# Optimization experiments

Measured on AMD Instinct MI355X. Metric: run time of the kernel, lower is better.

Reference implementation:

```python
import jax, jax.numpy as jnp
import numpy as np

N0, N1, N2 = 16384, 4096, 1024   # node counts at the 3 hierarchy levels
DEG = 16                          # avg degree -> E = N*DEG per level
OUT_CH = 4
GTD = 2048                        # global_token_dim


def _gcn(x, ei, w, b):
    # GCNConv: out = D^{-1/2} (A + I) D^{-1/2} (x @ W) + b
    n = x.shape[0]
    h = x @ w
    loop = jnp.arange(n, dtype=ei.dtype)
    src = jnp.concatenate([ei[0], loop])
    dst = jnp.concatenate([ei[1], loop])
    deg = jax.ops.segment_sum(jnp.ones(src.shape[0], h.dtype), dst, num_segments=n)
    dinv = jax.lax.rsqrt(jnp.maximum(deg, 1.0))   # deg >= 1 thanks to self loops
    coef = (dinv[src] * dinv[dst])[:, None]
    return jax.ops.segment_sum(h[src] * coef, dst, num_segments=n) + b


def _knn_interp(x, pos_src, pos_dst, k):
    # inverse-squared-distance weighted interpolation over k nearest sources
    d2 = (jnp.sum(pos_dst * pos_dst, -1, keepdims=True)
          + jnp.sum(pos_src * pos_src, -1)[None, :]
          - 2.0 * (pos_dst @ pos_src.T))          # (M, N) squared distances
    negd, idx = jax.lax.top_k(-d2, k)
    w = 1.0 / jnp.maximum(-negd, 1e-16)           # (M, k)
    return jnp.einsum('mk,mkc->mc', w, x[idx]) / jnp.sum(w, -1, keepdims=True)


def _bnorm(h, gamma, beta):
    # BatchNorm1d in training mode (batch statistics over nodes)
    mu = jnp.mean(h, 0)
    var = jnp.mean((h - mu) ** 2, 0)
    return (h - mu) * jax.lax.rsqrt(var + 1e-5) * gamma + beta


def _forward(fl, idx0, idx1, ei0, ei1, ei2):
    (x, pos,
     s1w0, s1b0, s1w1, s1b1, s1w2, s1b2,
     s2w0, s2b0, s2w1, s2b1, s2w2, s2b2,
     bw0, bb0, bw1, bb1, bw2, bb2,
     gw0, gb0, gw1, gb1, gw2, gb2, gg0, gbe0, gg1, gbe1,
     f2w0, f2b0, f2w1, f2b1, f2w2, f2b2,
     f1w0, f1b0, f1w1, f1b1, f1w2, f1b2,
     mw0, mb0, mw1, mb1) = fl
    relu = jax.nn.relu
    # SA1 (skip_pos_encoding=True): convs on full graph, then subsample by idx0
    h = relu(_gcn(x, ei0, s1w0, s1b0))
    h = relu(_gcn(h, ei0, s1w1, s1b1))
    h = relu(_gcn(h, ei0, s1w2, s1b2))
    x1, pos1 = h[idx0], pos[idx0]                 # (N1, 64)
    # SA2: concat pos, convs on level-1 graph, subsample by idx1
    h = jnp.concatenate([x1, pos1], 1)
    h = relu(_gcn(h, ei1, s2w0, s2b0))
    h = relu(_gcn(h, ei1, s2w1, s2b1))
    h = relu(_gcn(h, ei1, s2w2, s2b2))
    x2, pos2 = h[idx1], pos1[idx1]                # (N2, 128)
    # bottleneck (no subsample)
    h = jnp.concatenate([x2, pos2], 1)
    h = relu(_gcn(h, ei2, bw0, bb0))
    h = relu(_gcn(h, ei2, bw1, bb1))
    xb = relu(_gcn(h, ei2, bw2, bb2))             # (N2, 256)
    # GlobalSA: MLP(+BN) -> global max pool -> k=1 interp (broadcast, B=1) -> concat skip
    g = jnp.concatenate([x2, pos2], 1)
    g = relu(_bnorm(g @ gw0 + gb0, gg0, gbe0))
    g = relu(_bnorm(g @ gw1 + gb1, gg1, gbe1))
    g = g @ gw2 + gb2                             # (N2, GTD)
    gmax = jnp.max(g, 0, keepdims=True)
    h = jnp.concatenate([jnp.broadcast_to(gmax, (x2.shape[0], gmax.shape[1])), xb], 1)
    # FP2: knn-interpolate level2 -> level1, concat skip, convs on level-1 graph
    h = _knn_interp(h, pos2, pos1, 3)
    h = jnp.concatenate([h, x1], 1)               # (N1, GTD+256+64)
    h = relu(_gcn(h, ei1, f2w0, f2b0))
    h = relu(_gcn(h, ei1, f2w1, f2b1))
    h = relu(_gcn(h, ei1, f2w2, f2b2))
    # FP1: knn-interpolate level1 -> level0, concat raw features, convs on full graph
    h = _knn_interp(h, pos1, pos, 3)
    h = jnp.concatenate([h, x], 1)                # (N0, 518)
    h = relu(_gcn(h, ei0, f1w0, f1b0))
    h = relu(_gcn(h, ei0, f1w1, f1b1))
    h = relu(_gcn(h, ei0, f1w2, f1b2))            # (N0, 128)
    # final MLP (norm=None)
    return relu(h @ mw0 + mb0) @ mw1 + mb1        # (N0, OUT_CH)


def setup_inputs() -> dict:
    keys = iter(jax.random.split(jax.random.key(0), 64))
    def lin(i, o):
        return (jax.random.normal(next(keys), (i, o), jnp.float32) / np.float32(np.sqrt(i)),
                jnp.zeros((o,), jnp.float32))
    d = {}
    d['x'] = jax.random.normal(next(keys), (N0, 6), jnp.float32)
    d['pos'] = jax.random.uniform(next(keys), (N0, 3), jnp.float32)
    for nm, sp in [('sa1', [(6, 32), (32, 32), (32, 64)]),
                   ('sa2', [(67, 64), (64, 64), (64, 128)]),
                   ('bn', [(131, 128), (128, 128), (128, 256)])]:
        for j, (i, o) in enumerate(sp):
            d[nm + '_w' + str(j)], d[nm + '_b' + str(j)] = lin(i, o)
    for j, (i, o) in enumerate([(131, 512), (512, 1024), (1024, GTD)]):
        d['g_w' + str(j)], d['g_b' + str(j)] = lin(i, o)
    d['g_g0'] = jnp.ones((512,), jnp.float32); d['g_be0'] = jnp.zeros((512,), jnp.float32)
    d['g_g1'] = jnp.ones((1024,), jnp.float32); d['g_be1'] = jnp.zeros((1024,), jnp.float32)
    for nm, sp in [('fp2', [(GTD + 256 + 64, 1024), (1024, 1024), (1024, 512)]),
                   ('fp1', [(512 + 6, 256), (256, 256), (256, 128)])]:
        for j, (i, o) in enumerate(sp):
            d[nm + '_w' + str(j)], d[nm + '_b' + str(j)] = lin(i, o)
    d['m_w0'], d['m_b0'] = lin(128, 64)
    d['m_w1'], d['m_b1'] = lin(64, OUT_CH)
    d['idx0'] = jax.random.randint(next(keys), (N1,), 0, N0)
    d['idx1'] = jax.random.randint(next(keys), (N2,), 0, N1)
    d['ei0'] = jax.random.randint(next(keys), (2, N0 * DEG), 0, N0)
    d['ei1'] = jax.random.randint(next(keys), (2, N1 * DEG), 0, N1)
    d['ei2'] = jax.random.randint(next(keys), (2, N2 * DEG), 0, N2)
    return d


def reference(x, pos,
              sa1_w0, sa1_b0, sa1_w1, sa1_b1, sa1_w2, sa1_b2,
              sa2_w0, sa2_b0, sa2_w1, sa2_b1, sa2_w2, sa2_b2,
              bn_w0, bn_b0, bn_w1, bn_b1, bn_w2, bn_b2,
              g_w0, g_b0, g_w1, g_b1, g_w2, g_b2, g_g0, g_be0, g_g1, g_be1,
              fp2_w0, fp2_b0, fp2_w1, fp2_b1, fp2_w2, fp2_b2,
              fp1_w0, fp1_b0, fp1_w1, fp1_b1, fp1_w2, fp1_b2,
              m_w0, m_b0, m_w1, m_b1,
              idx0, idx1, ei0, ei1, ei2):
    fl = (x, pos,
          sa1_w0, sa1_b0, sa1_w1, sa1_b1, sa1_w2, sa1_b2,
          sa2_w0, sa2_b0, sa2_w1, sa2_b1, sa2_w2, sa2_b2,
          bn_w0, bn_b0, bn_w1, bn_b1, bn_w2, bn_b2,
          g_w0, g_b0, g_w1, g_b1, g_w2, g_b2, g_g0, g_be0, g_g1, g_be1,
          fp2_w0, fp2_b0, fp2_w1, fp2_b1, fp2_w2, fp2_b2,
          fp1_w0, fp1_b0, fp1_w1, fp1_b1, fp1_w2, fp1_b2,
          m_w0, m_b0, m_w1, m_b1)
    return _forward(fl, idx0, idx1, ei0, ei1, ei2)
```

## Files before the change

kernel.cpp:

```cpp
#include <hip/hip_runtime.h>
#include <hip/hip_bf16.h>

typedef __hip_bfloat16 bf16;
typedef __attribute__((ext_vector_type(8))) short bf8v;
typedef __attribute__((ext_vector_type(4))) float f32x4;

__device__ __forceinline__ float ldw(const void* p, long i, int isbf) {
    return isbf ? __bfloat162float(((const bf16*)p)[i]) : ((const float*)p)[i];
}
__device__ __forceinline__ unsigned short f2bf(float v) {
    bf16 h = __float2bfloat16(v);
    return *reinterpret_cast<unsigned short*>(&h);
}
__device__ __forceinline__ float bfu2f(unsigned short u) {
    return __uint_as_float((unsigned)u << 16);
}

__global__ void k_detect(const unsigned short* __restrict__ w, int n, int* __restrict__ flag) {
    __shared__ int cnt;
    if (threadIdx.x == 0) cnt = 0;
    __syncthreads();
    int bad = 0;
    for (int i = threadIdx.x; i < n; i += 256) {
        int e = (w[i] >> 7) & 0xFF;
        if (e == 0xFF || (e != 0 && (e < 64 || e > 190))) bad++;
    }
    atomicAdd(&cnt, bad);
    __syncthreads();
    if (threadIdx.x == 0) *flag = (cnt > n / 16) ? 0 : 1;
}

__global__ void k_cvt_in(const void* __restrict__ s, float* __restrict__ d, int n,
                         const int* __restrict__ flag) {
    int i = blockIdx.x * 256 + threadIdx.x;
    if (i < n) d[i] = ldw(s, i, *flag);
}
__global__ void k_out(const float* __restrict__ s, void* __restrict__ d, int n,
                      const int* __restrict__ flag) {
    int i = blockIdx.x * 256 + threadIdx.x;
    if (i < n) {
        if (*flag) ((bf16*)d)[i] = __float2bfloat16(s[i]);
        else       ((float*)d)[i] = s[i];
    }
}
__global__ void k_zero(float* __restrict__ d, int n) {
    int i = blockIdx.x * 256 + threadIdx.x;
    if (i < n) d[i] = 0.f;
}
__global__ void k_zero_i(int* __restrict__ d, int n) {
    int i = blockIdx.x * 256 + threadIdx.x;
    if (i < n) d[i] = 0;
}

__global__ void k_count(const int* __restrict__ dst, int* __restrict__ cnt, int E) {
    int i = blockIdx.x * 256 + threadIdx.x;
    if (i < E) atomicAdd(&cnt[dst[i]], 1);
}
__global__ void k_dinv_i(const int* __restrict__ cnt, float* __restrict__ dinv, int n) {
    int i = blockIdx.x * 256 + threadIdx.x;
    if (i < n) dinv[i] = rsqrtf((float)cnt[i] + 1.0f);
}
__global__ __launch_bounds__(1024) void k_scan(const int* __restrict__ cnt,
                                               int* __restrict__ offs, int n) {
    __shared__ int sm[1024];
    int t = threadIdx.x;
    int chunk = (n + 1023) >> 10;
    int b0 = t * chunk, b1 = min(b0 + chunk, n);
    int s = 0;
    for (int i = b0; i < b1; i++) s += cnt[i];
    sm[t] = s;
    __syncthreads();
    for (int o = 1; o < 1024; o <<= 1) {
        int v = (t >= o) ? sm[t - o] : 0;
        __syncthreads();
        sm[t] += v;
        __syncthreads();
    }
    int run = sm[t] - s;
    for (int i = b0; i < b1; i++) { offs[i] = run; run += cnt[i]; }
    if (t == 1023) offs[n] = sm[1023];
}
__global__ void k_fill(const int* __restrict__ src, const int* __restrict__ dst,
                       const int* __restrict__ offs, int* __restrict__ cur,
                       int* __restrict__ bkt, int E) {
    int e = blockIdx.x * 256 + threadIdx.x;
    if (e < E) {
        int d = dst[e];
        int p = atomicAdd(&cur[d], 1);
        bkt[offs[d] + p] = src[e];
    }
}

__global__ __launch_bounds__(256) void k_wt(const void* __restrict__ W, long woff,
                                            unsigned short* __restrict__ WTh,
                                            unsigned short* __restrict__ WTl,
                                            int K, int N, int Kpad,
                                            const int* __restrict__ flag) {
    __shared__ unsigned short th[32][33];
    __shared__ unsigned short tl[32][33];
    const int isbf = *flag;
    int n0 = blockIdx.x * 32, k0 = blockIdx.y * 32;
    int c = threadIdx.x & 31, r = threadIdx.x >> 5;
    #pragma unroll
    for (int u = 0; u < 4; u++) {
        int k = k0 + r + u * 8;
        float v = (k < K) ? ldw(W, woff + (long)k * N + n0 + c, isbf) : 0.f;
        unsigned short h = f2bf(v);
        th[r + u * 8][c] = h;
        tl[r + u * 8][c] = f2bf(v - bfu2f(h));
    }
    __syncthreads();
    #pragma unroll
    for (int u = 0; u < 4; u++) {
        int n = n0 + r + u * 8;
        WTh[(long)n * Kpad + k0 + c] = th[c][r + u * 8];
        WTl[(long)n * Kpad + k0 + c] = tl[c][r + u * 8];
    }
}

__global__ __launch_bounds__(256) void k_mm(
    const float* __restrict__ A, const void* __restrict__ Wt,
    const void* __restrict__ bias, const float* __restrict__ radd,
    const float* __restrict__ rsc, const float* __restrict__ rs,
    float* __restrict__ C, int M, int K, int N, long woff, int relu,
    const int* __restrict__ flag)
{
    __shared__ float As[2][16][68];
    __shared__ float Bs[2][16][68];
    const int isbf = *flag;
    const int tid = threadIdx.x;
    const int tx = tid & 15, ty = tid >> 4;
    const int bx = blockIdx.x, by = blockIdx.y;

    const int ar = tid >> 2, aq = (tid & 3) << 2;
    const long arow = (long)(by * 64 + ar) * K;
    const int bkk = tid >> 4, bn4 = (tid & 15) << 2;
    const int bcol0 = bx * 64 + bn4;

    float acc[4][4] = {};
    float4 pa, pb;

    auto loadAB = [&](int k0) {
        int kg = k0 + aq;
        pa.x = (kg + 0 < K) ? A[arow + kg + 0] : 0.f;
        pa.y = (kg + 1 < K) ? A[arow + kg + 1] : 0.f;
        pa.z = (kg + 2 < K) ? A[arow + kg + 2] : 0.f;
        pa.w = (kg + 3 < K) ? A[arow + kg + 3] : 0.f;
        int kb = k0 + bkk;
        pb = make_float4(0.f, 0.f, 0.f, 0.f);
        if (kb < K) {
            long base = woff + (long)kb * N + bcol0;
            if (bcol0 + 3 < N) {
                pb.x = ldw(Wt, base + 0, isbf); pb.y = ldw(Wt, base + 1, isbf);
                pb.z = ldw(Wt, base + 2, isbf); pb.w = ldw(Wt, base + 3, isbf);
            } else {
                if (bcol0 < N)     pb.x = ldw(Wt, base + 0, isbf);
                if (bcol0 + 1 < N) pb.y = ldw(Wt, base + 1, isbf);
                if (bcol0 + 2 < N) pb.z = ldw(Wt, base + 2, isbf);
            }
        }
    };
    auto storeAB = [&](int b) {
        As[b][aq + 0][ar] = pa.x;  As[b][aq + 1][ar] = pa.y;
        As[b][aq + 2][ar] = pa.z;  As[b][aq + 3][ar] = pa.w;
        *(float4*)&Bs[b][bkk][bn4] = pb;
    };

    loadAB(0);
    storeAB(0);
    __syncthreads();

    const int nk = (K + 15) >> 4;
    for (int t = 0; t < nk; t++) {
        const int cur = t & 1;
        const bool more = (t + 1 < nk);
        if (more) loadAB((t + 1) << 4);
        #pragma unroll
        for (int kk = 0; kk < 16; kk++) {
            float4 a = *(const float4*)&As[cur][kk][ty << 2];
            float4 b = *(const float4*)&Bs[cur][kk][tx << 2];
            float av[4] = {a.x, a.y, a.z, a.w};
            float bv[4] = {b.x, b.y, b.z, b.w};
            #pragma unroll
            for (int i = 0; i < 4; i++)
                #pragma unroll
                for (int j = 0; j < 4; j++)
                    acc[i][j] = fmaf(av[i], bv[j], acc[i][j]);
        }
        if (more) storeAB(cur ^ 1);
        __syncthreads();
    }

    const int col = bx * 64 + (tx << 2);
    #pragma unroll
    for (int i = 0; i < 4; i++) {
        int r = by * 64 + (ty << 2) + i;
        float m = rs ? rs[r] : 1.0f;
        float rr = rsc ? rsc[r] : 1.0f;
        float v[4];
        #pragma unroll
        for (int j = 0; j < 4; j++) {
            v[j] = acc[i][j] * m;
            int c = col + j;
            if (c < N) {
                if (bias) v[j] += ldw(bias, c, isbf);
                if (radd) v[j] += radd[c] * rr;
            }
            if (relu) v[j] = fmaxf(v[j], 0.f);
        }
        if (col + 3 < N) {
            float4 o = {v[0], v[1], v[2], v[3]};
            *(float4*)&C[(long)r * N + col] = o;
        } else {
            for (int j = 0; j < 4; j++)
                if (col + j < N) C[(long)r * N + col + j] = v[j];
        }
    }
}

__global__ __launch_bounds__(256, 4) void k_mmx(
    const float* __restrict__ A,
    const unsigned short* __restrict__ WTh, const unsigned short* __restrict__ WTl,
    const void* __restrict__ bias, const float* __restrict__ radd,
    const float* __restrict__ rsc, const float* __restrict__ rs,
    float* __restrict__ C, int M, int K, int Kpad, int N, int relu,
    const int* __restrict__ flag)
{
    __shared__ unsigned short Ash[64][72];
    __shared__ unsigned short Asl[64][72];
    __shared__ unsigned short Bsh[64][72];
    __shared__ unsigned short Bsl[64][72];
    const int tid = threadIdx.x;
    const int bx = blockIdx.x, by = blockIdx.y;
    const int lane = tid & 63, wid = tid >> 6;
    const int wr = wid >> 1, wc = wid & 1;
    const int lr = lane & 15, lg = lane >> 4;
    const int ar = tid >> 2, aq = (tid & 3) << 4;
    const long arow = (long)(by * 64 + ar) * K;
    const unsigned short* wrh = WTh + (long)(bx * 64 + ar) * Kpad;
    const unsigned short* wrl = WTl + (long)(bx * 64 + ar) * Kpad;

    f32x4 acc00 = {0,0,0,0}, acc01 = {0,0,0,0};
    f32x4 acc10 = {0,0,0,0}, acc11 = {0,0,0,0};
    bf8v pah0, pah1, pal0, pal1, pbh0, pbh1, pbl0, pbl1;

    auto ld = [&](int k0) {
        int kg = k0 + aq;
        float va[16];
        if (kg + 16 <= K) {
            if ((K & 3) == 0) {
                #pragma unroll
                for (int q = 0; q < 4; q++)
                    *(float4*)&va[4 * q] = *(const float4*)&A[arow + kg + 4 * q];
            } else if ((K & 1) == 0) {
                #pragma unroll
                for (int q = 0; q < 8; q++)
                    *(float2*)&va[2 * q] = *(const float2*)&A[arow + kg + 2 * q];
            } else {
                #pragma unroll
                for (int e = 0; e < 16; e++) va[e] = A[arow + kg + e];
            }
        } else {
            #pragma unroll
            for (int e = 0; e < 16; e++) va[e] = (kg + e < K) ? A[arow + kg + e] : 0.f;
        }
        #pragma unroll
        for (int e = 0; e < 8; e++) {
            unsigned short h = f2bf(va[e]);
            pah0[e] = (short)h;
            pal0[e] = (short)f2bf(va[e] - bfu2f(h));
        }
        #pragma unroll
        for (int e = 0; e < 8; e++) {
            unsigned short h = f2bf(va[8 + e]);
            pah1[e] = (short)h;
            pal1[e] = (short)f2bf(va[8 + e] - bfu2f(h));
        }
        pbh0 = *(const bf8v*)(wrh + kg);
        pbh1 = *(const bf8v*)(wrh + kg + 8);
        pbl0 = *(const bf8v*)(wrl + kg);
        pbl1 = *(const bf8v*)(wrl + kg + 8);
    };

    ld(0);
    for (int k0 = 0; k0 < K; k0 += 64) {
        __syncthreads();
        *(bf8v*)&Ash[ar][aq] = pah0;  *(bf8v*)&Ash[ar][aq + 8] = pah1;
        *(bf8v*)&Asl[ar][aq] = pal0;  *(bf8v*)&Asl[ar][aq + 8] = pal1;
        *(bf8v*)&Bsh[ar][aq] = pbh0;  *(bf8v*)&Bsh[ar][aq + 8] = pbh1;
        *(bf8v*)&Bsl[ar][aq] = pbl0;  *(bf8v*)&Bsl[ar][aq + 8] = pbl1;
        __syncthreads();
        if (k0 + 64 < K) ld(k0 + 64);
        #pragma unroll
        for (int ks = 0; ks < 2; ks++) {
            int kb = ks * 32 + lg * 8;
            bf8v a0h = *(const bf8v*)&Ash[wr * 32 + lr][kb];
            bf8v a1h = *(const bf8v*)&Ash[wr * 32 + 16 + lr][kb];
            bf8v a0l = *(const bf8v*)&Asl[wr * 32 + lr][kb];
            bf8v a1l = *(const bf8v*)&Asl[wr * 32 + 16 + lr][kb];
            bf8v b0h = *(const bf8v*)&Bsh[wc * 32 + lr][kb];
            bf8v b1h = *(const bf8v*)&Bsh[wc * 32 + 16 + lr][kb];
            bf8v b0l = *(const bf8v*)&Bsl[wc * 32 + lr][kb];
            bf8v b1l = *(const bf8v*)&Bsl[wc * 32 + 16 + lr][kb];
            acc00 = __builtin_amdgcn_mfma_f32_16x16x32_bf16(a0l, b0h, acc00, 0, 0, 0);
            acc00 = __builtin_amdgcn_mfma_f32_16x16x32_bf16(a0h, b0l, acc00, 0, 0, 0);
            acc00 = __builtin_amdgcn_mfma_f32_16x16x32_bf16(a0h, b0h, acc00, 0, 0, 0);
            acc01 = __builtin_amdgcn_mfma_f32_16x16x32_bf16(a0l, b1h, acc01, 0, 0, 0);
            acc01 = __builtin_amdgcn_mfma_f32_16x16x32_bf16(a0h, b1l, acc01, 0, 0, 0);
            acc01 = __builtin_amdgcn_mfma_f32_16x16x32_bf16(a0h, b1h, acc01, 0, 0, 0);
            acc10 = __builtin_amdgcn_mfma_f32_16x16x32_bf16(a1l, b0h, acc10, 0, 0, 0);
            acc10 = __builtin_amdgcn_mfma_f32_16x16x32_bf16(a1h, b0l, acc10, 0, 0, 0);
            acc10 = __builtin_amdgcn_mfma_f32_16x16x32_bf16(a1h, b0h, acc10, 0, 0, 0);
            acc11 = __builtin_amdgcn_mfma_f32_16x16x32_bf16(a1l, b1h, acc11, 0, 0, 0);
            acc11 = __builtin_amdgcn_mfma_f32_16x16x32_bf16(a1h, b1l, acc11, 0, 0, 0);
            acc11 = __builtin_amdgcn_mfma_f32_16x16x32_bf16(a1h, b1h, acc11, 0, 0, 0);
        }
    }

    const int isbf = *flag;
    const int rb = by * 64 + wr * 32, cb = bx * 64 + wc * 32;
    auto epi = [&](f32x4 a, int mf, int nf) {
        int col = cb + nf * 16 + lr;
        float bv = bias ? ldw(bias, col, isbf) : 0.f;
        float rv = radd ? radd[col] : 0.f;
        #pragma unroll
        for (int g = 0; g < 4; g++) {
            int row = rb + mf * 16 + lg * 4 + g;
            float v = a[g] * (rs ? rs[row] : 1.f) + bv
                    + rv * (rsc ? rsc[row] : 1.f);
            if (relu) v = fmaxf(v, 0.f);
            C[(long)row * N + col] = v;
        }
    };
    epi(acc00, 0, 0); epi(acc01, 0, 1); epi(acc10, 1, 0); epi(acc11, 1, 1);
}

__global__ __launch_bounds__(256) void k_aggr(const float* __restrict__ t,
    const int* __restrict__ offs, const int* __restrict__ bkt,
    const float* __restrict__ dinv, const void* __restrict__ bias,
    float* __restrict__ out, int n, int C, int relu, const int* __restrict__ flag)
{
    const int G = C >> 2;
    long i = blockIdx.x * 256L + threadIdx.x;
    if (i >= (long)n * G) return;
    int d = (int)(i / G), g = (int)(i % G);
    const float4* t4 = (const float4*)t;
    float4 acc = t4[(long)d * G + g];
    int o0 = offs[d], o1 = offs[d + 1];
    for (int j = o0; j < o1; j++) {
        int s = bkt[j];
        float4 v = t4[(long)s * G + g];
        acc.x += v.x; acc.y += v.y; acc.z += v.z; acc.w += v.w;
    }
    float dd = dinv[d];
    acc.x *= dd; acc.y *= dd; acc.z *= dd; acc.w *= dd;
    if (bias) {
        int isbf = *flag; int c = g << 2;
        acc.x += ldw(bias, c, isbf); acc.y += ldw(bias, c + 1, isbf);
        acc.z += ldw(bias, c + 2, isbf); acc.w += ldw(bias, c + 3, isbf);
    }
    if (relu) {
        acc.x = fmaxf(acc.x, 0.f); acc.y = fmaxf(acc.y, 0.f);
        acc.z = fmaxf(acc.z, 0.f); acc.w = fmaxf(acc.w, 0.f);
    }
    ((float4*)out)[(long)d * G + g] = acc;
}

__global__ void k_rowmul(float* __restrict__ h, const float* __restrict__ s, int n, int C) {
    long i = blockIdx.x * 256L + threadIdx.x;
    if (i < (long)n * C) h[i] *= s[i / C];
}
__global__ void k_sigacc(const int* __restrict__ src, const int* __restrict__ dst,
                         const float* __restrict__ dinv, float* __restrict__ sig, int E) {
    int e = blockIdx.x * 256 + threadIdx.x;
    if (e < E) atomicAdd(&sig[dst[e]], dinv[src[e]]);
}
__global__ void k_sigfin(float* __restrict__ sig, const float* __restrict__ dinv, int n) {
    int i = blockIdx.x * 256 + threadIdx.x;
    if (i < n) sig[i] = dinv[i] * (sig[i] + dinv[i]);
}
__global__ void k_rowvec_acc(const float* __restrict__ gmax, const void* __restrict__ W,
                             float* __restrict__ out, const int* __restrict__ flag) {
    int n = blockIdx.x * 256 + threadIdx.x;
    if (n >= 1024) return;
    const int isbf = *flag;
    int c0 = blockIdx.y * 128;
    float s = 0.f;
    for (int c = c0; c < c0 + 128; c++) s += gmax[c] * ldw(W, (long)c * 1024 + n, isbf);
    atomicAdd(&out[n], s);
}

__global__ __launch_bounds__(256) void k_bn(float* __restrict__ h, const void* __restrict__ gamma,
                                            const void* __restrict__ beta, int n, int C,
                                            const int* __restrict__ flag) {
    int c = blockIdx.x;
    int tid = threadIdx.x;
    __shared__ float sm[256];
    float v[4];
    float s = 0.f;
    #pragma unroll
    for (int u = 0; u < 4; u++) {
        int r = tid + u * 256;
        v[u] = (r < n) ? h[(long)r * C + c] : 0.f;
        s += v[u];
    }
    sm[tid] = s; __syncthreads();
    for (int o = 128; o > 0; o >>= 1) { if (tid < o) sm[tid] += sm[tid + o]; __syncthreads(); }
    float mu = sm[0] / n;
    __syncthreads();
    float s2 = 0.f;
    #pragma unroll
    for (int u = 0; u < 4; u++) {
        int r = tid + u * 256;
        if (r < n) { float d = v[u] - mu; s2 += d * d; }
    }
    sm[tid] = s2; __syncthreads();
    for (int o = 128; o > 0; o >>= 1) { if (tid < o) sm[tid] += sm[tid + o]; __syncthreads(); }
    float var = sm[0] / n;
    float rsq = rsqrtf(var + 1e-5f);
    float g = ldw(gamma, c, *flag), be = ldw(beta, c, *flag);
    #pragma unroll
    for (int u = 0; u < 4; u++) {
        int r = tid + u * 256;
        if (r < n) h[(long)r * C + c] = fmaxf((v[u] - mu) * rsq * g + be, 0.f);
    }
}

__global__ __launch_bounds__(256) void k_cmax(const float* __restrict__ h, float* __restrict__ out) {
    __shared__ float sm[256];
    int coff = threadIdx.x & 63, rq = threadIdx.x >> 6;
    int c = blockIdx.x * 64 + coff;
    float m = -3.0e38f;
    for (int r = rq; r < 1024; r += 4) m = fmaxf(m, h[(long)r * 2048 + c]);
    sm[threadIdx.x] = m;
    __syncthreads();
    if (rq == 0) {
        m = fmaxf(fmaxf(sm[coff], sm[64 + coff]), fmaxf(sm[128 + coff], sm[192 + coff]));
        out[c] = m;
    }
}

__global__ void k_gather(const float* __restrict__ src, const int* __restrict__ idx,
                         float* __restrict__ dst, int n, int ncol, int ss, int ds, int doff) {
    long i = blockIdx.x * 256L + threadIdx.x;
    if (i < (long)n * ncol) {
        int r = (int)(i / ncol), c = (int)(i % ncol);
        dst[(long)r * ds + doff + c] = src[(long)idx[r] * ss + c];
    }
}
__global__ void k_copy(const float* __restrict__ src, float* __restrict__ dst,
                       int n, int ncol, int ss, int ds, int doff) {
    long i = blockIdx.x * 256L + threadIdx.x;
    if (i < (long)n * ncol) {
        int r = (int)(i / ncol), c = (int)(i % ncol);
        dst[(long)r * ds + doff + c] = src[(long)r * ss + c];
    }
}

__device__ __forceinline__ bool knn_better(float d, int i, float D, int I) {
    return d < D || (d == D && i < I);
}
__global__ __launch_bounds__(256) void k_knn_w(const float* __restrict__ pdst,
                                               const float* __restrict__ psrc,
                                               int M, int Ns,
                                               int* __restrict__ kidx, float* __restrict__ kw) {
    int wid = (blockIdx.x * 256 + threadIdx.x) >> 6;
    int lane = threadIdx.x & 63;
    if (wid >= M) return;
    float x = pdst[wid * 3], y = pdst[wid * 3 + 1], z = pdst[wid * 3 + 2];
    float nd = x * x + y * y + z * z;
    float bd0 = 3.4e38f, bd1 = 3.4e38f, bd2 = 3.4e38f;
    int bi0 = 0x7fffffff, bi1 = 0x7fffffff, bi2 = 0x7fffffff;
    for (int s = lane; s < Ns; s += 64) {
        float sx = psrc[3 * s], sy = psrc[3 * s + 1], sz = psrc[3 * s + 2];
        float ns = sx * sx + sy * sy + sz * sz;
        float d2 = nd + ns - 2.0f * (x * sx + y * sy + z * sz);
        if (d2 < bd2) {
            if (d2 < bd0)      { bd2 = bd1; bi2 = bi1; bd1 = bd0; bi1 = bi0; bd0 = d2; bi0 = s; }
            else if (d2 < bd1) { bd2 = bd1; bi2 = bi1; bd1 = d2; bi1 = s; }
            else               { bd2 = d2; bi2 = s; }
        }
    }
    #pragma unroll
    for (int off = 32; off >= 1; off >>= 1) {
        float od0 = __shfl_xor(bd0, off, 64); int oi0 = __shfl_xor(bi0, off, 64);
        float od1 = __shfl_xor(bd1, off, 64); int oi1 = __shfl_xor(bi1, off, 64);
        float od2 = __shfl_xor(bd2, off, 64); int oi2 = __shfl_xor(bi2, off, 64);
        float dq[3] = {od0, od1, od2}; int iq[3] = {oi0, oi1, oi2};
        #pragma unroll
        for (int q = 0; q < 3; q++) {
            float dd = dq[q]; int ii = iq[q];
            if (knn_better(dd, ii, bd0, bi0))      { bd2 = bd1; bi2 = bi1; bd1 = bd0; bi1 = bi0; bd0 = dd; bi0 = ii; }
            else if (knn_better(dd, ii, bd1, bi1)) { bd2 = bd1; bi2 = bi1; bd1 = dd; bi1 = ii; }
            else if (knn_better(dd, ii, bd2, bi2)) { bd2 = dd; bi2 = ii; }
        }
    }
    if (lane == 0) {
        kidx[wid * 3] = bi0; kidx[wid * 3 + 1] = bi1; kidx[wid * 3 + 2] = bi2;
        kw[wid * 3]     = 1.0f / fmaxf(bd0, 1e-16f);
        kw[wid * 3 + 1] = 1.0f / fmaxf(bd1, 1e-16f);
        kw[wid * 3 + 2] = 1.0f / fmaxf(bd2, 1e-16f);
    }
}

__global__ void k_knn_apply4(const float* __restrict__ h, const int* __restrict__ kidx,
                             const float* __restrict__ kw, float* __restrict__ out,
                             int M, int C, int ds) {
    const int G = C >> 2;
    long i = blockIdx.x * 256L + threadIdx.x;
    if (i >= (long)M * G) return;
    int r = (int)(i / G), g = (int)(i % G);
    int i0 = kidx[r * 3], i1 = kidx[r * 3 + 1], i2 = kidx[r * 3 + 2];
    float w0 = kw[r * 3], w1 = kw[r * 3 + 1], w2 = kw[r * 3 + 2];
    float inv = 1.0f / (w0 + w1 + w2);
    const float4* h4 = (const float4*)h;
    float4 a = h4[(long)i0 * G + g], b = h4[(long)i1 * G + g], c = h4[(long)i2 * G + g];
    float4 o;
    o.x = (w0 * a.x + w1 * b.x + w2 * c.x) * inv;
    o.y = (w0 * a.y + w1 * b.y + w2 * c.y) * inv;
    o.z = (w0 * a.z + w1 * b.z + w2 * c.z) * inv;
    o.w = (w0 * a.w + w1 * b.w + w2 * c.w) * inv;
    *(float4*)&out[(long)r * ds + (g << 2)] = o;
}
__global__ void k_knn_apply2(const float* __restrict__ h, const int* __restrict__ kidx,
                             const float* __restrict__ kw, float* __restrict__ out,
                             int M, int C, int ds) {
    const int G = C >> 1;
    long i = blockIdx.x * 256L + threadIdx.x;
    if (i >= (long)M * G) return;
    int r = (int)(i / G), g = (int)(i % G);
    int i0 = kidx[r * 3], i1 = kidx[r * 3 + 1], i2 = kidx[r * 3 + 2];
    float w0 = kw[r * 3], w1 = kw[r * 3 + 1], w2 = kw[r * 3 + 2];
    float inv = 1.0f / (w0 + w1 + w2);
    const float2* h2 = (const float2*)h;
    float2 a = h2[(long)i0 * G + g], b = h2[(long)i1 * G + g], c = h2[(long)i2 * G + g];
    float2 o;
    o.x = (w0 * a.x + w1 * b.x + w2 * c.x) * inv;
    o.y = (w0 * a.y + w1 * b.y + w2 * c.y) * inv;
    *(float2*)&out[(long)r * ds + (g << 1)] = o;
}

extern "C" void kernel_launch(void* const* d_in, const int* in_sizes, int n_in,
                              void* d_out, int out_size, void* d_ws, size_t ws_size,
                              hipStream_t stream) {
    const int N0 = 16384, N1 = 4096, N2 = 1024;
    const int E0 = in_sizes[48] / 2, E1 = in_sizes[49] / 2, E2 = in_sizes[50] / 2;

    const int* idx0 = (const int*)d_in[46];
    const int* idx1 = (const int*)d_in[47];
    const int* ei0  = (const int*)d_in[48];
    const int* ei1  = (const int*)d_in[49];
    const int* ei2  = (const int*)d_in[50];

    float* W = (float*)d_ws;
    size_t off = 0;
    auto alloc = [&](size_t nf) { float* p = W + off; off += (nf + 63) & ~(size_t)63; return p; };
    auto allocU = [&](size_t nu) { return (unsigned short*)alloc((nu + 1) / 2); };
    float* P     = alloc(4194304);
    float* Q     = alloc(4194304);
    float* CAT   = alloc(8486912);
    float* xf    = alloc(98304);
    float* posf  = alloc(49152);
    float* pos1  = alloc(12288);
    float* pos2  = alloc(3072);
    float* dinv0 = alloc(16384);
    float* dinv1 = alloc(4096);
    float* dinv2 = alloc(1024);
    float* x1    = alloc(262144);
    float* c2    = alloc(134144);
    float* xb    = alloc(262144);
    float* gmaxb = alloc(2048);
    float* rowv  = alloc(1024);
    float* sigb  = alloc(4096);
    float* kwb   = alloc(49152);
    int*   kib   = (int*)alloc(49152);
    int*   flg   = (int*)alloc(64);
    int*   cntb  = (int*)alloc(16384);
    int*   offs0 = (int*)alloc(16448);
    int*   offs1 = (int*)alloc(4160);
    int*   offs2 = (int*)alloc(1088);
    int*   bkt0  = (int*)alloc(E0);
    int*   bkt1  = (int*)alloc(E1);
    int*   bkt2  = (int*)alloc(E2);

    struct WtPair { unsigned short *h, *l; int Kp; };
    auto mkwt = [&](size_t n, int Kp) {
        WtPair p; p.h = allocU(n); p.l = allocU(n); p.Kp = Kp; return p;
    };
    WtPair wt6  = mkwt(64 * 64, 64);
    WtPair wt8  = mkwt(64 * 128, 128);
    WtPair wt10 = mkwt(64 * 64, 64);
    WtPair wt12 = mkwt(128 * 64, 64);
    WtPair wt14 = mkwt(128 * 192, 192);
    WtPair wt16 = mkwt(128 * 128, 128);
    WtPair wt18 = mkwt(256 * 128, 128);
    WtPair wt20 = mkwt(512 * 192, 192);
    WtPair wt22 = mkwt(1024 * 512, 512);
    WtPair wt24 = mkwt(2048 * 1024, 1024);
    WtPair wt30 = mkwt(1024 * 320, 320);
    WtPair wt32 = mkwt(1024 * 1024, 1024);
    WtPair wt34 = mkwt(512 * 1024, 1024);
    WtPair wt36 = mkwt(256 * 576, 576);
    WtPair wt38 = mkwt(256 * 256, 256);
    WtPair wt40 = mkwt(128 * 256, 256);
    WtPair wt42 = mkwt(64 * 128, 128);

    const bool usex = (off * sizeof(float)) <= ws_size;

    auto g1 = [](long n) { return dim3((unsigned)((n + 255) / 256)); };

    auto mm = [&](const float* Ain, int iw, int ib, const float* radd, const float* rsc,
                  const float* rs, float* out, int M_, int K_, int N_, long woff, int relu) {
        dim3 g((N_ + 63) / 64, M_ / 64);
        k_mm<<<g, 256, 0, stream>>>(Ain, d_in[iw], ib >= 0 ? d_in[ib] : nullptr,
                                    radd, rsc, rs, out, M_, K_, N_, woff, relu, flg);
    };
    auto mmx = [&](const float* Ain, int iw, int ib, const float* radd, const float* rsc,
                   const float* rs, float* out, int M_, int K_, int N_, long woff, int relu,
                   const WtPair& wp) {
        if (usex) {
            dim3 g(N_ / 64, M_ / 64);
            k_mmx<<<g, 256, 0, stream>>>(Ain, wp.h, wp.l,
                                         ib >= 0 ? d_in[ib] : nullptr,
                                         radd, rsc, rs, out, M_, K_, wp.Kp, N_, relu, flg);
        } else {
            mm(Ain, iw, ib, radd, rsc, rs, out, M_, K_, N_, woff, relu);
        }
    };
    auto gcnx = [&](const float* Ain, int n, int K, int iw, int ib, int C,
                    const int* offs, const int* bkt, const float* dinv, float* t, float* out,
                    const WtPair& wp) {
        mmx(Ain, iw, -1, nullptr, nullptr, dinv, t, n, K, C, 0, 0, wp);
        k_aggr<<<g1((long)n * (C >> 2)), 256, 0, stream>>>(t, offs, bkt, dinv, d_in[ib],
                                                           out, n, C, 1, flg);
    };
    auto gcn = [&](const float* Ain, int n, int K, int iw, int ib, int C,
                   const int* offs, const int* bkt, const float* dinv, float* t, float* out) {
        mm(Ain, iw, -1, nullptr, nullptr, dinv, t, n, K, C, 0, 0);
        k_aggr<<<g1((long)n * (C >> 2)), 256, 0, stream>>>(t, offs, bkt, dinv, d_in[ib],
                                                           out, n, C, 1, flg);
    };
    auto csr = [&](const int* ei, int E, int n, int* offs, int* bkt, float* dinv) {
        k_zero_i<<<g1(n), 256, 0, stream>>>(cntb, n);
        k_count<<<g1(E), 256, 0, stream>>>(ei + E, cntb, E);
        k_dinv_i<<<g1(n), 256, 0, stream>>>(cntb, dinv, n);
        k_scan<<<1, 1024, 0, stream>>>(cntb, offs, n);
        k_zero_i<<<g1(n), 256, 0, stream>>>(cntb, n);
        k_fill<<<g1(E), 256, 0, stream>>>(ei, ei + E, offs, cntb, bkt, E);
    };
    auto wtk = [&](int iw, long woff, int K_, int N_, const WtPair& wp) {
        if (!usex) return;
        dim3 g(N_ / 32, wp.Kp / 32);
        k_wt<<<g, 256, 0, stream>>>(d_in[iw], woff, wp.h, wp.l, K_, N_, wp.Kp, flg);
    };

    k_detect<<<1, 256, 0, stream>>>((const unsigned short*)d_in[2], in_sizes[2], flg);
    k_cvt_in<<<g1(N0 * 6), 256, 0, stream>>>(d_in[0], xf, N0 * 6, flg);
    k_cvt_in<<<g1(N0 * 3), 256, 0, stream>>>(d_in[1], posf, N0 * 3, flg);
    csr(ei0, E0, N0, offs0, bkt0, dinv0);
    csr(ei1, E1, N1, offs1, bkt1, dinv1);
    csr(ei2, E2, N2, offs2, bkt2, dinv2);
    wtk(6, 0, 32, 64, wt6);
    wtk(8, 0, 67, 64, wt8);
    wtk(10, 0, 64, 64, wt10);
    wtk(12, 0, 64, 128, wt12);
    wtk(14, 0, 131, 128, wt14);
    wtk(16, 0, 128, 128, wt16);
    wtk(18, 0, 128, 256, wt18);
    wtk(20, 0, 131, 512, wt20);
    wtk(22, 0, 512, 1024, wt22);
    wtk(24, 0, 1024, 2048, wt24);
    wtk(30, 2048L * 1024L, 320, 1024, wt30);
    wtk(32, 0, 1024, 1024, wt32);
    wtk(34, 0, 1024, 512, wt34);
    wtk(36, 0, 518, 256, wt36);
    wtk(38, 0, 256, 256, wt38);
    wtk(40, 0, 256, 128, wt40);
    wtk(42, 0, 128, 64, wt42);

    gcn(xf, N0, 6, 2, 3, 32, offs0, bkt0, dinv0, P, Q);
    gcn(Q, N0, 32, 4, 5, 32, offs0, bkt0, dinv0, P, Q);
    gcnx(Q, N0, 32, 6, 7, 64, offs0, bkt0, dinv0, P, Q, wt6);
    k_gather<<<g1((long)N1 * 64), 256, 0, stream>>>(Q, idx0, x1, N1, 64, 64, 64, 0);
    k_gather<<<g1((long)N1 * 3), 256, 0, stream>>>(posf, idx0, pos1, N1, 3, 3, 3, 0);

    k_copy<<<g1((long)N1 * 64), 256, 0, stream>>>(x1, P, N1, 64, 64, 67, 0);
    k_copy<<<g1((long)N1 * 3), 256, 0, stream>>>(pos1, P, N1, 3, 3, 67, 64);
    gcnx(P, N1, 67, 8, 9, 64, offs1, bkt1, dinv1, Q, P, wt8);
    gcnx(P, N1, 64, 10, 11, 64, offs1, bkt1, dinv1, Q, P, wt10);
    gcnx(P, N1, 64, 12, 13, 128, offs1, bkt1, dinv1, Q, P, wt12);
    k_gather<<<g1((long)N2 * 128), 256, 0, stream>>>(P, idx1, c2, N2, 128, 128, 131, 0);
    k_gather<<<g1((long)N2 * 3), 256, 0, stream>>>(pos1, idx1, pos2, N2, 3, 3, 3, 0);
    k_copy<<<g1((long)N2 * 3), 256, 0, stream>>>(pos2, c2, N2, 3, 3, 131, 128);

    gcnx(c2, N2, 131, 14, 15, 128, offs2, bkt2, dinv2, P, Q, wt14);
    gcnx(Q, N2, 128, 16, 17, 128, offs2, bkt2, dinv2, P, Q, wt16);
    gcnx(Q, N2, 128, 18, 19, 256, offs2, bkt2, dinv2, P, xb, wt18);

    mmx(c2, 20, 21, nullptr, nullptr, nullptr, P, N2, 131, 512, 0, 0, wt20);
    k_bn<<<dim3(512), 256, 0, stream>>>(P, d_in[26], d_in[27], N2, 512, flg);
    mmx(P, 22, 23, nullptr, nullptr, nullptr, Q, N2, 512, 1024, 0, 0, wt22);
    k_bn<<<dim3(1024), 256, 0, stream>>>(Q, d_in[28], d_in[29], N2, 1024, flg);
    mmx(Q, 24, 25, nullptr, nullptr, nullptr, P, N2, 1024, 2048, 0, 0, wt24);
    k_cmax<<<dim3(32), 256, 0, stream>>>(P, gmaxb);

    k_zero<<<g1(1024), 256, 0, stream>>>(rowv, 1024);
    k_rowvec_acc<<<dim3(4, 16), 256, 0, stream>>>(gmaxb, d_in[30], rowv, flg);
    k_knn_w<<<g1((long)N1 * 64), 256, 0, stream>>>(pos1, pos2, N1, N2, kib, kwb);
    k_knn_apply4<<<g1((long)N1 * 64), 256, 0, stream>>>(xb, kib, kwb, CAT, N1, 256, 320);
    k_copy<<<g1((long)N1 * 64), 256, 0, stream>>>(x1, CAT, N1, 64, 64, 320, 256);
    k_rowmul<<<g1((long)N1 * 320), 256, 0, stream>>>(CAT, dinv1, N1, 320);
    k_aggr<<<g1((long)N1 * 80), 256, 0, stream>>>(CAT, offs1, bkt1, dinv1, nullptr,
                                                  P, N1, 320, 0, flg);
    k_zero<<<g1(N1), 256, 0, stream>>>(sigb, N1);
    k_sigacc<<<g1(E1), 256, 0, stream>>>(ei1, ei1 + E1, dinv1, sigb, E1);
    k_sigfin<<<g1(N1), 256, 0, stream>>>(sigb, dinv1, N1);
    mmx(P, 30, 31, rowv, sigb, nullptr, Q, N1, 320, 1024, 2048L * 1024L, 1, wt30);
    gcnx(Q, N1, 1024, 32, 33, 1024, offs1, bkt1, dinv1, P, Q, wt32);
    gcnx(Q, N1, 1024, 34, 35, 512, offs1, bkt1, dinv1, P, Q, wt34);

    k_knn_w<<<g1((long)N0 * 64), 256, 0, stream>>>(posf, pos1, N0, N1, kib, kwb);
    k_knn_apply2<<<g1((long)N0 * 256), 256, 0, stream>>>(Q, kib, kwb, CAT, N0, 512, 518);
    k_copy<<<g1((long)N0 * 6), 256, 0, stream>>>(xf, CAT, N0, 6, 6, 518, 512);
    gcnx(CAT, N0, 518, 36, 37, 256, offs0, bkt0, dinv0, P, Q, wt36);
    gcnx(Q, N0, 256, 38, 39, 256, offs0, bkt0, dinv0, P, CAT, wt38);
    gcnx(CAT, N0, 256, 40, 41, 128, offs0, bkt0, dinv0, P, Q, wt40);

    mmx(Q, 42, 43, nullptr, nullptr, nullptr, P, N0, 128, 64, 0, 1, wt42);
    mm(P, 44, 45, nullptr, nullptr, nullptr, xf, N0, 64, 4, 0, 0);
    k_out<<<g1(N0 * 4), 256, 0, stream>>>(xf, d_out, N0 * 4, flg);
}
```

Baseline: 1.168 ms.

## Pack source positions with norms for kNN, unroll aggregation, fuse row scaling

Source positions are pre-packed into float4 holding xyz plus squared norm. The kNN search then does one vector load and one FMA chain per candidate, processes two candidates per iteration, and adds the destination norm back only when computing the final weights. The neighbour-aggregation loop is unrolled by four to keep more independent gathers in flight. The separate row-scaling pass is folded into the knn_apply4 and copy kernels. This adds two small packing launches, and rounding in the distance ranking changes slightly.

```diff
diff --git a/kernel.cpp b/kernel.cpp
--- a/kernel.cpp
+++ b/kernel.cpp
@@ -50,6 +50,14 @@
 __global__ void k_zero_i(int* __restrict__ d, int n) {
     int i = blockIdx.x * 256 + threadIdx.x;
     if (i < n) d[i] = 0;
+}
+__global__ void k_pack4(const float* __restrict__ p, float4* __restrict__ o, int n) {
+    int i = blockIdx.x * 256 + threadIdx.x;
+    if (i < n) {
+        float x = p[3 * i], y = p[3 * i + 1], z = p[3 * i + 2];
+        float4 v = {x, y, z, fmaf(x, x, fmaf(y, y, z * z))};
+        o[i] = v;
+    }
 }
 
 __global__ void k_count(const int* __restrict__ dst, int* __restrict__ cnt, int E) {
@@ -347,7 +355,19 @@
     const float4* t4 = (const float4*)t;
     float4 acc = t4[(long)d * G + g];
     int o0 = offs[d], o1 = offs[d + 1];
-    for (int j = o0; j < o1; j++) {
+    int j = o0;
+    for (; j + 3 < o1; j += 4) {
+        int s0 = bkt[j], s1 = bkt[j + 1], s2 = bkt[j + 2], s3 = bkt[j + 3];
+        float4 v0 = t4[(long)s0 * G + g];
+        float4 v1 = t4[(long)s1 * G + g];
+        float4 v2 = t4[(long)s2 * G + g];
+        float4 v3 = t4[(long)s3 * G + g];
+        acc.x += v0.x; acc.y += v0.y; acc.z += v0.z; acc.w += v0.w;
+        acc.x += v1.x; acc.y += v1.y; acc.z += v1.z; acc.w += v1.w;
+        acc.x += v2.x; acc.y += v2.y; acc.z += v2.z; acc.w += v2.w;
+        acc.x += v3.x; acc.y += v3.y; acc.z += v3.z; acc.w += v3.w;
+    }
+    for (; j < o1; j++) {
         int s = bkt[j];
         float4 v = t4[(long)s * G + g];
         acc.x += v.x; acc.y += v.y; acc.z += v.z; acc.w += v.w;
@@ -366,10 +386,6 @@
     ((float4*)out)[(long)d * G + g] = acc;
 }
 
-__global__ void k_rowmul(float* __restrict__ h, const float* __restrict__ s, int n, int C) {
-    long i = blockIdx.x * 256L + threadIdx.x;
-    if (i < (long)n * C) h[i] *= s[i / C];
-}
 __global__ void k_sigacc(const int* __restrict__ src, const int* __restrict__ dst,
                          const float* __restrict__ dinv, float* __restrict__ sig, int E) {
     int e = blockIdx.x * 256 + threadIdx.x;
@@ -449,11 +465,14 @@
     }
 }
 __global__ void k_copy(const float* __restrict__ src, float* __restrict__ dst,
+                       const float* __restrict__ rmul,
                        int n, int ncol, int ss, int ds, int doff) {
     long i = blockIdx.x * 256L + threadIdx.x;
     if (i < (long)n * ncol) {
         int r = (int)(i / ncol), c = (int)(i % ncol);
-        dst[(long)r * ds + doff + c] = src[(long)r * ss + c];
+        float v = src[(long)r * ss + c];
+        if (rmul) v *= rmul[r];
+        dst[(long)r * ds + doff + c] = v;
     }
 }
 
@@ -461,25 +480,36 @@
     return d < D || (d == D && i < I);
 }
 __global__ __launch_bounds__(256) void k_knn_w(const float* __restrict__ pdst,
-                                               const float* __restrict__ psrc,
+                                               const float4* __restrict__ psrc4,
                                                int M, int Ns,
                                                int* __restrict__ kidx, float* __restrict__ kw) {
     int wid = (blockIdx.x * 256 + threadIdx.x) >> 6;
     int lane = threadIdx.x & 63;
     if (wid >= M) return;
     float x = pdst[wid * 3], y = pdst[wid * 3 + 1], z = pdst[wid * 3 + 2];
-    float nd = x * x + y * y + z * z;
+    float nd = fmaf(x, x, fmaf(y, y, z * z));
     float bd0 = 3.4e38f, bd1 = 3.4e38f, bd2 = 3.4e38f;
     int bi0 = 0x7fffffff, bi1 = 0x7fffffff, bi2 = 0x7fffffff;
-    for (int s = lane; s < Ns; s += 64) {
-        float sx = psrc[3 * s], sy = psrc[3 * s + 1], sz = psrc[3 * s + 2];
-        float ns = sx * sx + sy * sy + sz * sz;
-        float d2 = nd + ns - 2.0f * (x * sx + y * sy + z * sz);
-        if (d2 < bd2) {
-            if (d2 < bd0)      { bd2 = bd1; bi2 = bi1; bd1 = bd0; bi1 = bi0; bd0 = d2; bi0 = s; }
-            else if (d2 < bd1) { bd2 = bd1; bi2 = bi1; bd1 = d2; bi1 = s; }
-            else               { bd2 = d2; bi2 = s; }
-        }
+    auto ins = [&](float r, int s) {
+        if (r < bd2) {
+            if (r < bd0)      { bd2 = bd1; bi2 = bi1; bd1 = bd0; bi1 = bi0; bd0 = r; bi0 = s; }
+            else if (r < bd1) { bd2 = bd1; bi2 = bi1; bd1 = r; bi1 = s; }
+            else              { bd2 = r; bi2 = s; }
+        }
+    };
+    int s = lane;
+    for (; s + 64 < Ns; s += 128) {
+        float4 q0 = psrc4[s];
+        float4 q1 = psrc4[s + 64];
+        float r0 = fmaf(-2.f, fmaf(x, q0.x, fmaf(y, q0.y, z * q0.z)), q0.w);
+        float r1 = fmaf(-2.f, fmaf(x, q1.x, fmaf(y, q1.y, z * q1.z)), q1.w);
+        ins(r0, s);
+        ins(r1, s + 64);
+    }
+    for (; s < Ns; s += 64) {
+        float4 q = psrc4[s];
+        float r = fmaf(-2.f, fmaf(x, q.x, fmaf(y, q.y, z * q.z)), q.w);
+        ins(r, s);
     }
     #pragma unroll
     for (int off = 32; off >= 1; off >>= 1) {
@@ -497,14 +527,15 @@
     }
     if (lane == 0) {
         kidx[wid * 3] = bi0; kidx[wid * 3 + 1] = bi1; kidx[wid * 3 + 2] = bi2;
-        kw[wid * 3]     = 1.0f / fmaxf(bd0, 1e-16f);
-        kw[wid * 3 + 1] = 1.0f / fmaxf(bd1, 1e-16f);
-        kw[wid * 3 + 2] = 1.0f / fmaxf(bd2, 1e-16f);
+        kw[wid * 3]     = 1.0f / fmaxf(nd + bd0, 1e-16f);
+        kw[wid * 3 + 1] = 1.0f / fmaxf(nd + bd1, 1e-16f);
+        kw[wid * 3 + 2] = 1.0f / fmaxf(nd + bd2, 1e-16f);
     }
 }
 
 __global__ void k_knn_apply4(const float* __restrict__ h, const int* __restrict__ kidx,
-                             const float* __restrict__ kw, float* __restrict__ out,
+                             const float* __restrict__ kw, const float* __restrict__ rmul,
+                             float* __restrict__ out,
                              int M, int C, int ds) {
     const int G = C >> 2;
     long i = blockIdx.x * 256L + threadIdx.x;
@@ -520,6 +551,10 @@
     o.y = (w0 * a.y + w1 * b.y + w2 * c.y) * inv;
     o.z = (w0 * a.z + w1 * b.z + w2 * c.z) * inv;
     o.w = (w0 * a.w + w1 * b.w + w2 * c.w) * inv;
+    if (rmul) {
+        float dd = rmul[r];
+        o.x *= dd; o.y *= dd; o.z *= dd; o.w *= dd;
+    }
     *(float4*)&out[(long)r * ds + (g << 2)] = o;
 }
 __global__ void k_knn_apply2(const float* __restrict__ h, const int* __restrict__ kidx,
@@ -563,6 +598,8 @@
     float* posf  = alloc(49152);
     float* pos1  = alloc(12288);
     float* pos2  = alloc(3072);
+    float* pos1p = alloc(16384);
+    float* pos2p = alloc(4096);
     float* dinv0 = alloc(16384);
     float* dinv1 = alloc(4096);
     float* dinv2 = alloc(1024);
@@ -684,14 +721,14 @@
     k_gather<<<g1((long)N1 * 64), 256, 0, stream>>>(Q, idx0, x1, N1, 64, 64, 64, 0);
     k_gather<<<g1((long)N1 * 3), 256, 0, stream>>>(posf, idx0, pos1, N1, 3, 3, 3, 0);
 
-    k_copy<<<g1((long)N1 * 64), 256, 0, stream>>>(x1, P, N1, 64, 64, 67, 0);
-    k_copy<<<g1((long)N1 * 3), 256, 0, stream>>>(pos1, P, N1, 3, 3, 67, 64);
+    k_copy<<<g1((long)N1 * 64), 256, 0, stream>>>(x1, P, nullptr, N1, 64, 64, 67, 0);
+    k_copy<<<g1((long)N1 * 3), 256, 0, stream>>>(pos1, P, nullptr, N1, 3, 3, 67, 64);
     gcnx(P, N1, 67, 8, 9, 64, offs1, bkt1, dinv1, Q, P, wt8);
     gcnx(P, N1, 64, 10, 11, 64, offs1, bkt1, dinv1, Q, P, wt10);
     gcnx(P, N1, 64, 12, 13, 128, offs1, bkt1, dinv1, Q, P, wt12);
     k_gather<<<g1((long)N2 * 128), 256, 0, stream>>>(P, idx1, c2, N2, 128, 128, 131, 0);
     k_gather<<<g1((long)N2 * 3), 256, 0, stream>>>(pos1, idx1, pos2, N2, 3, 3, 3, 0);
-    k_copy<<<g1((long)N2 * 3), 256, 0, stream>>>(pos2, c2, N2, 3, 3, 131, 128);
+    k_copy<<<g1((long)N2 * 3), 256, 0, stream>>>(pos2, c2, nullptr, N2, 3, 3, 131, 128);
 
     gcnx(c2, N2, 131, 14, 15, 128, offs2, bkt2, dinv2, P, Q, wt14);
     gcnx(Q, N2, 128, 16, 17, 128, offs2, bkt2, dinv2, P, Q, wt16);
@@ -706,10 +743,11 @@
 
     k_zero<<<g1(1024), 256, 0, stream>>>(rowv, 1024);
     k_rowvec_acc<<<dim3(4, 16), 256, 0, stream>>>(gmaxb, d_in[30], rowv, flg);
-    k_knn_w<<<g1((long)N1 * 64), 256, 0, stream>>>(pos1, pos2, N1, N2, kib, kwb);
-    k_knn_apply4<<<g1((long)N1 * 64), 256, 0, stream>>>(xb, kib, kwb, CAT, N1, 256, 320);
-    k_copy<<<g1((long)N1 * 64), 256, 0, stream>>>(x1, CAT, N1, 64, 64, 320, 256);
-    k_rowmul<<<g1((long)N1 * 320), 256, 0, stream>>>(CAT, dinv1, N1, 320);
+    k_pack4<<<g1(N1), 256, 0, stream>>>(pos1, (float4*)pos1p, N1);
+    k_pack4<<<g1(N2), 256, 0, stream>>>(pos2, (float4*)pos2p, N2);
+    k_knn_w<<<g1((long)N1 * 64), 256, 0, stream>>>(pos1, (const float4*)pos2p, N1, N2, kib, kwb);
+    k_knn_apply4<<<g1((long)N1 * 64), 256, 0, stream>>>(xb, kib, kwb, dinv1, CAT, N1, 256, 320);
+    k_copy<<<g1((long)N1 * 64), 256, 0, stream>>>(x1, CAT, dinv1, N1, 64, 64, 320, 256);
     k_aggr<<<g1((long)N1 * 80), 256, 0, stream>>>(CAT, offs1, bkt1, dinv1, nullptr,
                                                   P, N1, 320, 0, flg);
     k_zero<<<g1(N1), 256, 0, stream>>>(sigb, N1);
@@ -719,9 +757,9 @@
     gcnx(Q, N1, 1024, 32, 33, 1024, offs1, bkt1, dinv1, P, Q, wt32);
     gcnx(Q, N1, 1024, 34, 35, 512, offs1, bkt1, dinv1, P, Q, wt34);
 
-    k_knn_w<<<g1((long)N0 * 64), 256, 0, stream>>>(posf, pos1, N0, N1, kib, kwb);
+    k_knn_w<<<g1((long)N0 * 64), 256, 0, stream>>>(posf, (const float4*)pos1p, N0, N1, kib, kwb);
     k_knn_apply2<<<g1((long)N0 * 256), 256, 0, stream>>>(Q, kib, kwb, CAT, N0, 512, 518);
-    k_copy<<<g1((long)N0 * 6), 256, 0, stream>>>(xf, CAT, N0, 6, 6, 518, 512);
+    k_copy<<<g1((long)N0 * 6), 256, 0, stream>>>(xf, CAT, nullptr, N0, 6, 6, 518, 512);
     gcnx(CAT, N0, 518, 36, 37, 256, offs0, bkt0, dinv0, P, Q, wt36);
     gcnx(Q, N0, 256, 38, 39, 256, offs0, bkt0, dinv0, P, CAT, wt38);
     gcnx(CAT, N0, 256, 40, 41, 128, offs0, bkt0, dinv0, P, Q, wt40);
```

New measurement: 1.167 ms. Within noise of the previous version (-0.1%).
